# Kernel tuning notes

Measured on AMD Instinct MI355X. Metric: run time of the kernel, lower is better.

## Reference

```python
import jax, jax.numpy as jnp
import numpy as np

ALPHA = 0.1        # self.alpha in the torch module
NUM_CLASSES = 10   # predict_acc hardcodes range(10)


def _sqdist(x, centers):
    # Faithful to sum((x - c)**2, -1) but computed via the gemm identity to
    # avoid materializing the (N, K, D) broadcast the torch code creates.
    x2 = jnp.sum(x * x, axis=1, keepdims=True)          # [N, 1]
    c2 = jnp.sum(centers * centers, axis=1)             # [K]
    d = x2 + c2[None, :] - 2.0 * (x @ centers.T)        # [N, K]
    return jnp.maximum(d, 0.0)                          # clamp fp round-off


def _predict_acc(distance, y):
    n = distance.shape[0]
    y_p = jnp.argmin(distance, axis=1)                  # index[1][:, 0]
    # counts[i, c] = #points assigned to cluster i (only i < 10 matter) with label c
    onehot_cluster = (y_p[:, None] == jnp.arange(NUM_CLASSES)[None, :]).astype(jnp.float32)  # [N, 10]
    onehot_label = (y[:, None] == jnp.arange(NUM_CLASSES)[None, :]).astype(jnp.float32)      # [N, 10]
    counts = onehot_cluster.T @ onehot_label            # [10, 10]
    used = jnp.zeros((NUM_CLASSES,), dtype=bool)
    correct = jnp.float32(0.0)
    for i in range(NUM_CLASSES):
        bin_i = counts[i]
        has_points = jnp.sum(bin_i) > 0                 # empty bincount -> 'continue'
        label = jnp.argmax(bin_i)                       # first max index, like where(bin==max)[0][0]
        # quchong: recursively zero already-used labels == argmax with used masked out
        masked = jnp.where(used, 0.0, bin_i)
        label = jnp.where(used[label], jnp.argmax(masked), label)
        correct = correct + jnp.where(has_points, bin_i[label], 0.0)
        used = jnp.where(has_points, used.at[label].set(True), used)
    return correct / jnp.float32(n)


def setup_inputs() -> dict:
    key = jax.random.key(0)
    kx, ky, kc = jax.random.split(key, 3)
    N, K, D = 262144, 256, 64
    x = jax.random.normal(kx, (N, D), dtype=jnp.float32)
    y = jax.random.randint(ky, (N,), 0, 10, dtype=jnp.int64)
    centers = jax.random.normal(kc, (K, D), dtype=jnp.float32)
    return {"x": x, "y": y, "centers": centers}


def reference(x, y, centers):
    distance = _sqdist(x, centers)                      # caldis, op='l2'
    # calwei: exp(-alpha*log(d+1)) then row-normalize
    we = jnp.exp(-ALPHA * jnp.log1p(distance))
    weight = we / jnp.sum(we, axis=1, keepdims=True)
    loss = jnp.sum(weight * distance)                   # calloss
    acc = _predict_acc(distance, y)
    return (loss, acc)
```

## Files before the change

### kernel.cpp

```cpp
#include <hip/hip_runtime.h>

#define ALPHA 0.1f
#define NUM_CLASSES 10

typedef __attribute__((ext_vector_type(8))) short bf16x8;
typedef __attribute__((ext_vector_type(4))) float f32x4;


__device__ __forceinline__ unsigned pack2(float a, float b) {
    return (__float_as_uint(b) & 0xFFFF0000u) | (__float_as_uint(a) >> 16);
}
__device__ __forceinline__ float truncbf(float a) {
    return __uint_as_float(__float_as_uint(a) & 0xFFFF0000u);
}


__global__ __launch_bounds__(256) void prep_kernel(
    const float* __restrict__ centers,
    unsigned int* __restrict__ ctpk,
    float* __restrict__ c2,
    float* __restrict__ loss_acc,
    unsigned int* __restrict__ counts)
{
    const int k = threadIdx.x;
    const int cg = k >> 6, ct = (k >> 4) & 3, r = k & 15;

    float cv[64];
    float s = 0.f;
    const float4* crow = (const float4*)(centers + k * 64);
#pragma unroll
    for (int j4 = 0; j4 < 16; ++j4) {
        float4 v = crow[j4];
        cv[j4 * 4 + 0] = v.x; cv[j4 * 4 + 1] = v.y;
        cv[j4 * 4 + 2] = v.z; cv[j4 * 4 + 3] = v.w;
        s += v.x * v.x + v.y * v.y + v.z * v.z + v.w * v.w;
    }
    c2[k] = s;

    uint4* out4 = (uint4*)ctpk;
#pragma unroll
    for (int f = 0; f < 4; ++f) {
#pragma unroll
        for (int q = 0; q < 4; ++q) {
            const int cbase = (f & 1) * 32 + q * 8;
            unsigned wv[4];
#pragma unroll
            for (int j2 = 0; j2 < 4; ++j2) {
                float a = cv[cbase + j2 * 2], b = cv[cbase + j2 * 2 + 1];
                if (f >= 2) { a = a - truncbf(a); b = b - truncbf(b); }
                wv[j2] = pack2(a, b);
            }
            const int lane = q * 16 + r;
            out4[((cg * 4 + ct) * 4 + f) * 64 + lane] =
                make_uint4(wv[0], wv[1], wv[2], wv[3]);
        }
    }
    if (k < NUM_CLASSES * NUM_CLASSES) counts[k] = 0u;
    if (k == 0) loss_acc[0] = 0.f;
}


__global__ __launch_bounds__(256, 2) void dist_kernel(
    const float* __restrict__ x,
    const int*   __restrict__ y,
    const unsigned int* __restrict__ ctpk,
    const float* __restrict__ c2g,
    float* __restrict__ loss_acc,
    unsigned int* __restrict__ counts,
    int NT)
{
    __shared__ float    comb_swe[4][64];
    __shared__ float    comb_swd[4][64];
    __shared__ unsigned comb_best[4][64];

    const int tid  = threadIdx.x;
    const int cg   = tid >> 6;
    const int lane = tid & 63;
    const int q    = lane >> 4;
    const int r    = lane & 15;

    bf16x8 af[4][4];
    const uint4* cp4 = (const uint4*)ctpk;
#pragma unroll
    for (int ct = 0; ct < 4; ++ct)
#pragma unroll
        for (int f = 0; f < 4; ++f) {
            union { uint4 u; bf16x8 v; } tmp;
            tmp.u = cp4[((cg * 4 + ct) * 4 + f) * 64 + lane];
            af[ct][f] = tmp.v;
        }

    float c2r[4][4];
#pragma unroll
    for (int ct = 0; ct < 4; ++ct) {
        float4 v = *(const float4*)(c2g + cg * 64 + ct * 16 + q * 4);
        c2r[ct][0] = v.x; c2r[ct][1] = v.y; c2r[ct][2] = v.z; c2r[ct][3] = v.w;
    }

    float loss_local = 0.f;

    for (int t = blockIdx.x; t < NT; t += gridDim.x) {
        bf16x8 bh0[4], bh1[4], bl0[4], bl1[4];
        float x2v[4];
#pragma unroll
        for (int pt = 0; pt < 4; ++pt) {
            const int row = t * 64 + pt * 16 + r;
            const float4* X = (const float4*)(x + (size_t)row * 64);
            float4 v0 = X[q * 2], v1 = X[q * 2 + 1];
            float4 v2 = X[8 + q * 2], v3 = X[9 + q * 2];

            float p = v0.x * v0.x;
            p = fmaf(v0.y, v0.y, p); p = fmaf(v0.z, v0.z, p); p = fmaf(v0.w, v0.w, p);
            p = fmaf(v1.x, v1.x, p); p = fmaf(v1.y, v1.y, p); p = fmaf(v1.z, v1.z, p); p = fmaf(v1.w, v1.w, p);
            p = fmaf(v2.x, v2.x, p); p = fmaf(v2.y, v2.y, p); p = fmaf(v2.z, v2.z, p); p = fmaf(v2.w, v2.w, p);
            p = fmaf(v3.x, v3.x, p); p = fmaf(v3.y, v3.y, p); p = fmaf(v3.z, v3.z, p); p = fmaf(v3.w, v3.w, p);
            p += __shfl_xor(p, 16);
            p += __shfl_xor(p, 32);
            x2v[pt] = p;

            union { bf16x8 v; unsigned u[4]; } h0, h1, l0, l1;
            h0.u[0] = pack2(v0.x, v0.y); h0.u[1] = pack2(v0.z, v0.w);
            h0.u[2] = pack2(v1.x, v1.y); h0.u[3] = pack2(v1.z, v1.w);
            h1.u[0] = pack2(v2.x, v2.y); h1.u[1] = pack2(v2.z, v2.w);
            h1.u[2] = pack2(v3.x, v3.y); h1.u[3] = pack2(v3.z, v3.w);
            l0.u[0] = pack2(v0.x - truncbf(v0.x), v0.y - truncbf(v0.y));
            l0.u[1] = pack2(v0.z - truncbf(v0.z), v0.w - truncbf(v0.w));
            l0.u[2] = pack2(v1.x - truncbf(v1.x), v1.y - truncbf(v1.y));
            l0.u[3] = pack2(v1.z - truncbf(v1.z), v1.w - truncbf(v1.w));
            l1.u[0] = pack2(v2.x - truncbf(v2.x), v2.y - truncbf(v2.y));
            l1.u[1] = pack2(v2.z - truncbf(v2.z), v2.w - truncbf(v2.w));
            l1.u[2] = pack2(v3.x - truncbf(v3.x), v3.y - truncbf(v3.y));
            l1.u[3] = pack2(v3.z - truncbf(v3.z), v3.w - truncbf(v3.w));
            bh0[pt] = h0.v; bh1[pt] = h1.v; bl0[pt] = l0.v; bl1[pt] = l1.v;
        }

        f32x4 acc[4][4];
#pragma unroll
        for (int ct = 0; ct < 4; ++ct)
#pragma unroll
            for (int pt = 0; pt < 4; ++pt) acc[ct][pt] = (f32x4){0.f, 0.f, 0.f, 0.f};

#pragma unroll
        for (int ct = 0; ct < 4; ++ct)
#pragma unroll
            for (int pt = 0; pt < 4; ++pt) {
                f32x4 a = acc[ct][pt];
                a = __builtin_amdgcn_mfma_f32_16x16x32_bf16(af[ct][0], bh0[pt], a, 0, 0, 0);
                a = __builtin_amdgcn_mfma_f32_16x16x32_bf16(af[ct][1], bh1[pt], a, 0, 0, 0);
                a = __builtin_amdgcn_mfma_f32_16x16x32_bf16(af[ct][2], bh0[pt], a, 0, 0, 0);
                a = __builtin_amdgcn_mfma_f32_16x16x32_bf16(af[ct][3], bh1[pt], a, 0, 0, 0);
                a = __builtin_amdgcn_mfma_f32_16x16x32_bf16(af[ct][0], bl0[pt], a, 0, 0, 0);
                a = __builtin_amdgcn_mfma_f32_16x16x32_bf16(af[ct][1], bl1[pt], a, 0, 0, 0);
                acc[ct][pt] = a;
            }

#pragma unroll
        for (int pt = 0; pt < 4; ++pt) {
            float swe = 0.f, swd = 0.f;
            unsigned best = 0xFFFFFFFFu;
            const float x2p = x2v[pt];
#pragma unroll
            for (int ct = 0; ct < 4; ++ct) {
#pragma unroll
                for (int reg = 0; reg < 4; ++reg) {
                    float d = fmaf(-2.f, acc[ct][pt][reg], x2p + c2r[ct][reg]);
                    d = fmaxf(d, 0.f);
                    const unsigned kid = (unsigned)(cg * 64 + ct * 16 + q * 4 + reg);
                    unsigned u = (__float_as_uint(d) & 0xFFFFFF00u) | kid;
                    best = min(best, u);
                    float wg = exp2f(-ALPHA * __log2f(1.f + d));
                    swe += wg;
                    swd = fmaf(wg, d, swd);
                }
            }
            swe += __shfl_xor(swe, 16); swe += __shfl_xor(swe, 32);
            swd += __shfl_xor(swd, 16); swd += __shfl_xor(swd, 32);
            best = min(best, (unsigned)__shfl_xor((int)best, 16));
            best = min(best, (unsigned)__shfl_xor((int)best, 32));
            if (q == 0) {
                comb_swe[cg][pt * 16 + r] = swe;
                comb_swd[cg][pt * 16 + r] = swd;
                comb_best[cg][pt * 16 + r] = best;
            }
        }
        __syncthreads();

        if (tid < 64) {
            float SWE = comb_swe[0][tid], SWD = comb_swd[0][tid];
            unsigned BEST = comb_best[0][tid];
#pragma unroll
            for (int g = 1; g < 4; ++g) {
                SWE += comb_swe[g][tid];
                SWD += comb_swd[g][tid];
                BEST = min(BEST, comb_best[g][tid]);
            }
            loss_local += SWD / SWE;
            const unsigned bk = BEST & 0xFFu;
            if (bk < NUM_CLASSES) {
                const int lbl = y[t * 64 + tid];
                atomicAdd(&counts[bk * NUM_CLASSES + lbl], 1u);
            }
        }
        __syncthreads();
    }

    if (cg == 0) {
        float v = loss_local;
#pragma unroll
        for (int o = 32; o > 0; o >>= 1) v += __shfl_down(v, o);
        if (lane == 0) atomicAdd(loss_acc, v);
    }
}


__global__ void finalize_kernel(
    const float* __restrict__ loss_acc,
    const unsigned int* __restrict__ counts,
    float* __restrict__ out,
    int N)
{
    if (threadIdx.x == 0 && blockIdx.x == 0) {
        float c[NUM_CLASSES][NUM_CLASSES];
        for (int i = 0; i < NUM_CLASSES; ++i)
            for (int j = 0; j < NUM_CLASSES; ++j)
                c[i][j] = (float)counts[i * NUM_CLASSES + j];

        bool used[NUM_CLASSES];
        for (int i = 0; i < NUM_CLASSES; ++i) used[i] = false;

        float correct = 0.f;
        for (int i = 0; i < NUM_CLASSES; ++i) {
            float rowsum = 0.f;
            for (int j = 0; j < NUM_CLASSES; ++j) rowsum += c[i][j];
            bool has_points = rowsum > 0.f;

            int label = 0;
            float mx = c[i][0];
            for (int j = 1; j < NUM_CLASSES; ++j)
                if (c[i][j] > mx) { mx = c[i][j]; label = j; }

            if (used[label]) {
                float mm = used[0] ? 0.f : c[i][0];
                int l2 = 0;
                for (int j = 1; j < NUM_CLASSES; ++j) {
                    float v = used[j] ? 0.f : c[i][j];
                    if (v > mm) { mm = v; l2 = j; }
                }
                label = l2;
            }

            if (has_points) {
                correct += c[i][label];
                used[label] = true;
            }
        }
        out[0] = loss_acc[0];
        out[1] = correct / (float)N;
    }
}


extern "C" void kernel_launch(void* const* d_in, const int* in_sizes, int n_in,
                              void* d_out, int out_size, void* d_ws, size_t ws_size,
                              hipStream_t stream)
{
    const float* x       = (const float*)d_in[0];
    const int*   y       = (const int*)d_in[1];
    const float* centers = (const float*)d_in[2];
    float* out = (float*)d_out;

    const int N  = in_sizes[0] / 64;
    const int NT = N / 64;

    unsigned int* ctpk   = (unsigned int*)d_ws;
    float* c2            = (float*)((char*)d_ws + 65536);
    float* loss          = (float*)((char*)d_ws + 66560);
    unsigned int* counts = (unsigned int*)((char*)d_ws + 66564);

    prep_kernel<<<1, 256, 0, stream>>>(centers, ctpk, c2, loss, counts);

    int grid = 512;
    if (grid > NT) grid = NT;
    dist_kernel<<<grid, 256, 0, stream>>>(x, y, ctpk, c2, loss, counts, NT);

    finalize_kernel<<<1, 64, 0, stream>>>(loss, counts, out, N);
}
```

Baseline: 161.0 us.

## Fuse center prep into distance kernel and split centers across eight waves

Drops the separate prep kernel. Each block now computes the center norms and the bf16 hi/lo center fragments itself, and counters are zeroed with a memset. Blocks grow to 512 threads: eight waves each own 32 centers, while four waves load and split the x tile and stage it through shared memory for all eight. The aim is to remove a launch, cut per-wave register pressure and raise occupancy. The cost is that every block re-reads the centers, and there is an extra LDS round trip plus a barrier per tile.

```diff
diff --git a/kernel.cpp b/kernel.cpp
--- a/kernel.cpp
+++ b/kernel.cpp
@@ -15,96 +15,75 @@
 }
 
 
-__global__ __launch_bounds__(256) void prep_kernel(
-    const float* __restrict__ centers,
-    unsigned int* __restrict__ ctpk,
-    float* __restrict__ c2,
-    float* __restrict__ loss_acc,
-    unsigned int* __restrict__ counts)
-{
-    const int k = threadIdx.x;
-    const int cg = k >> 6, ct = (k >> 4) & 3, r = k & 15;
-
-    float cv[64];
-    float s = 0.f;
-    const float4* crow = (const float4*)(centers + k * 64);
-#pragma unroll
-    for (int j4 = 0; j4 < 16; ++j4) {
-        float4 v = crow[j4];
-        cv[j4 * 4 + 0] = v.x; cv[j4 * 4 + 1] = v.y;
-        cv[j4 * 4 + 2] = v.z; cv[j4 * 4 + 3] = v.w;
-        s += v.x * v.x + v.y * v.y + v.z * v.z + v.w * v.w;
-    }
-    c2[k] = s;
-
-    uint4* out4 = (uint4*)ctpk;
-#pragma unroll
-    for (int f = 0; f < 4; ++f) {
-#pragma unroll
-        for (int q = 0; q < 4; ++q) {
-            const int cbase = (f & 1) * 32 + q * 8;
-            unsigned wv[4];
-#pragma unroll
-            for (int j2 = 0; j2 < 4; ++j2) {
-                float a = cv[cbase + j2 * 2], b = cv[cbase + j2 * 2 + 1];
-                if (f >= 2) { a = a - truncbf(a); b = b - truncbf(b); }
-                wv[j2] = pack2(a, b);
-            }
-            const int lane = q * 16 + r;
-            out4[((cg * 4 + ct) * 4 + f) * 64 + lane] =
-                make_uint4(wv[0], wv[1], wv[2], wv[3]);
-        }
-    }
-    if (k < NUM_CLASSES * NUM_CLASSES) counts[k] = 0u;
-    if (k == 0) loss_acc[0] = 0.f;
-}
-
-
-__global__ __launch_bounds__(256, 2) void dist_kernel(
+__global__ __launch_bounds__(512, 4) void dist_kernel(
     const float* __restrict__ x,
     const int*   __restrict__ y,
-    const unsigned int* __restrict__ ctpk,
-    const float* __restrict__ c2g,
+    const float* __restrict__ centers,
     float* __restrict__ loss_acc,
     unsigned int* __restrict__ counts,
     int NT)
 {
-    __shared__ float    comb_swe[4][64];
-    __shared__ float    comb_swd[4][64];
-    __shared__ unsigned comb_best[4][64];
+    __shared__ __align__(16) char bstage[4 * 4 * 64 * 16];
+    __shared__ float x2s[64];
+    __shared__ float c2s[256];
+    __shared__ float    comb_swe[8][64];
+    __shared__ float    comb_swd[8][64];
+    __shared__ unsigned comb_best[8][64];
 
     const int tid  = threadIdx.x;
-    const int cg   = tid >> 6;
+    const int w    = tid >> 6;
     const int lane = tid & 63;
     const int q    = lane >> 4;
     const int r    = lane & 15;
 
-    bf16x8 af[4][4];
-    const uint4* cp4 = (const uint4*)ctpk;
-#pragma unroll
-    for (int ct = 0; ct < 4; ++ct)
-#pragma unroll
-        for (int f = 0; f < 4; ++f) {
-            union { uint4 u; bf16x8 v; } tmp;
-            tmp.u = cp4[((cg * 4 + ct) * 4 + f) * 64 + lane];
-            af[ct][f] = tmp.v;
-        }
-
-    float c2r[4][4];
-#pragma unroll
-    for (int ct = 0; ct < 4; ++ct) {
-        float4 v = *(const float4*)(c2g + cg * 64 + ct * 16 + q * 4);
+    if (tid < 256) {
+        const float4* crow = (const float4*)(centers + tid * 64);
+        float s = 0.f;
+#pragma unroll
+        for (int j = 0; j < 16; ++j) {
+            float4 v = crow[j];
+            s = fmaf(v.x, v.x, s); s = fmaf(v.y, v.y, s);
+            s = fmaf(v.z, v.z, s); s = fmaf(v.w, v.w, s);
+        }
+        c2s[tid] = s;
+    }
+
+    bf16x8 af[2][4];
+#pragma unroll
+    for (int ct = 0; ct < 2; ++ct) {
+        const int row = w * 32 + ct * 16 + r;
+        const float4* C = (const float4*)(centers + (size_t)row * 64);
+        float4 v0 = C[q * 2], v1 = C[q * 2 + 1];
+        float4 v2 = C[8 + q * 2], v3 = C[9 + q * 2];
+        union { bf16x8 v; unsigned u[4]; } h0, h1, l0, l1;
+        h0.u[0] = pack2(v0.x, v0.y); h0.u[1] = pack2(v0.z, v0.w);
+        h0.u[2] = pack2(v1.x, v1.y); h0.u[3] = pack2(v1.z, v1.w);
+        h1.u[0] = pack2(v2.x, v2.y); h1.u[1] = pack2(v2.z, v2.w);
+        h1.u[2] = pack2(v3.x, v3.y); h1.u[3] = pack2(v3.z, v3.w);
+        l0.u[0] = pack2(v0.x - truncbf(v0.x), v0.y - truncbf(v0.y));
+        l0.u[1] = pack2(v0.z - truncbf(v0.z), v0.w - truncbf(v0.w));
+        l0.u[2] = pack2(v1.x - truncbf(v1.x), v1.y - truncbf(v1.y));
+        l0.u[3] = pack2(v1.z - truncbf(v1.z), v1.w - truncbf(v1.w));
+        l1.u[0] = pack2(v2.x - truncbf(v2.x), v2.y - truncbf(v2.y));
+        l1.u[1] = pack2(v2.z - truncbf(v2.z), v2.w - truncbf(v2.w));
+        l1.u[2] = pack2(v3.x - truncbf(v3.x), v3.y - truncbf(v3.y));
+        l1.u[3] = pack2(v3.z - truncbf(v3.z), v3.w - truncbf(v3.w));
+        af[ct][0] = h0.v; af[ct][1] = h1.v; af[ct][2] = l0.v; af[ct][3] = l1.v;
+    }
+    __syncthreads();
+
+    float c2r[2][4];
+#pragma unroll
+    for (int ct = 0; ct < 2; ++ct) {
+        float4 v = *(const float4*)(c2s + w * 32 + ct * 16 + q * 4);
         c2r[ct][0] = v.x; c2r[ct][1] = v.y; c2r[ct][2] = v.z; c2r[ct][3] = v.w;
     }
 
     float loss_local = 0.f;
 
     for (int t = blockIdx.x; t < NT; t += gridDim.x) {
-        bf16x8 bh0[4], bh1[4], bl0[4], bl1[4];
-        float x2v[4];
-#pragma unroll
-        for (int pt = 0; pt < 4; ++pt) {
-            const int row = t * 64 + pt * 16 + r;
+        if (w < 4) {
+            const int row = t * 64 + w * 16 + r;
             const float4* X = (const float4*)(x + (size_t)row * 64);
             float4 v0 = X[q * 2], v1 = X[q * 2 + 1];
             float4 v2 = X[8 + q * 2], v3 = X[9 + q * 2];
@@ -116,9 +95,9 @@
             p = fmaf(v3.x, v3.x, p); p = fmaf(v3.y, v3.y, p); p = fmaf(v3.z, v3.z, p); p = fmaf(v3.w, v3.w, p);
             p += __shfl_xor(p, 16);
             p += __shfl_xor(p, 32);
-            x2v[pt] = p;
-
-            union { bf16x8 v; unsigned u[4]; } h0, h1, l0, l1;
+            if (q == 0) x2s[w * 16 + r] = p;
+
+            union { bf16x8 v; uint4 u4; unsigned u[4]; } h0, h1, l0, l1;
             h0.u[0] = pack2(v0.x, v0.y); h0.u[1] = pack2(v0.z, v0.w);
             h0.u[2] = pack2(v1.x, v1.y); h0.u[3] = pack2(v1.z, v1.w);
             h1.u[0] = pack2(v2.x, v2.y); h1.u[1] = pack2(v2.z, v2.w);
@@ -131,41 +110,44 @@
             l1.u[1] = pack2(v2.z - truncbf(v2.z), v2.w - truncbf(v2.w));
             l1.u[2] = pack2(v3.x - truncbf(v3.x), v3.y - truncbf(v3.y));
             l1.u[3] = pack2(v3.z - truncbf(v3.z), v3.w - truncbf(v3.w));
-            bh0[pt] = h0.v; bh1[pt] = h1.v; bl0[pt] = l0.v; bl1[pt] = l1.v;
-        }
-
-        f32x4 acc[4][4];
-#pragma unroll
-        for (int ct = 0; ct < 4; ++ct)
-#pragma unroll
-            for (int pt = 0; pt < 4; ++pt) acc[ct][pt] = (f32x4){0.f, 0.f, 0.f, 0.f};
-
-#pragma unroll
-        for (int ct = 0; ct < 4; ++ct)
-#pragma unroll
-            for (int pt = 0; pt < 4; ++pt) {
-                f32x4 a = acc[ct][pt];
-                a = __builtin_amdgcn_mfma_f32_16x16x32_bf16(af[ct][0], bh0[pt], a, 0, 0, 0);
-                a = __builtin_amdgcn_mfma_f32_16x16x32_bf16(af[ct][1], bh1[pt], a, 0, 0, 0);
-                a = __builtin_amdgcn_mfma_f32_16x16x32_bf16(af[ct][2], bh0[pt], a, 0, 0, 0);
-                a = __builtin_amdgcn_mfma_f32_16x16x32_bf16(af[ct][3], bh1[pt], a, 0, 0, 0);
-                a = __builtin_amdgcn_mfma_f32_16x16x32_bf16(af[ct][0], bl0[pt], a, 0, 0, 0);
-                a = __builtin_amdgcn_mfma_f32_16x16x32_bf16(af[ct][1], bl1[pt], a, 0, 0, 0);
-                acc[ct][pt] = a;
-            }
+            *(uint4*)(bstage + (((w * 4 + 0) * 64 + lane) << 4)) = h0.u4;
+            *(uint4*)(bstage + (((w * 4 + 1) * 64 + lane) << 4)) = h1.u4;
+            *(uint4*)(bstage + (((w * 4 + 2) * 64 + lane) << 4)) = l0.u4;
+            *(uint4*)(bstage + (((w * 4 + 3) * 64 + lane) << 4)) = l1.u4;
+        }
+        __syncthreads();
 
 #pragma unroll
         for (int pt = 0; pt < 4; ++pt) {
+            union { uint4 u4; bf16x8 v; } b0, b1, b2, b3;
+            b0.u4 = *(const uint4*)(bstage + (((pt * 4 + 0) * 64 + lane) << 4));
+            b1.u4 = *(const uint4*)(bstage + (((pt * 4 + 1) * 64 + lane) << 4));
+            b2.u4 = *(const uint4*)(bstage + (((pt * 4 + 2) * 64 + lane) << 4));
+            b3.u4 = *(const uint4*)(bstage + (((pt * 4 + 3) * 64 + lane) << 4));
+            const float x2p = x2s[pt * 16 + r];
+
+            f32x4 acc[2];
+#pragma unroll
+            for (int ct = 0; ct < 2; ++ct) {
+                f32x4 a = (f32x4){0.f, 0.f, 0.f, 0.f};
+                a = __builtin_amdgcn_mfma_f32_16x16x32_bf16(af[ct][0], b0.v, a, 0, 0, 0);
+                a = __builtin_amdgcn_mfma_f32_16x16x32_bf16(af[ct][1], b1.v, a, 0, 0, 0);
+                a = __builtin_amdgcn_mfma_f32_16x16x32_bf16(af[ct][2], b0.v, a, 0, 0, 0);
+                a = __builtin_amdgcn_mfma_f32_16x16x32_bf16(af[ct][3], b1.v, a, 0, 0, 0);
+                a = __builtin_amdgcn_mfma_f32_16x16x32_bf16(af[ct][0], b2.v, a, 0, 0, 0);
+                a = __builtin_amdgcn_mfma_f32_16x16x32_bf16(af[ct][1], b3.v, a, 0, 0, 0);
+                acc[ct] = a;
+            }
+
             float swe = 0.f, swd = 0.f;
             unsigned best = 0xFFFFFFFFu;
-            const float x2p = x2v[pt];
-#pragma unroll
-            for (int ct = 0; ct < 4; ++ct) {
+#pragma unroll
+            for (int ct = 0; ct < 2; ++ct) {
 #pragma unroll
                 for (int reg = 0; reg < 4; ++reg) {
-                    float d = fmaf(-2.f, acc[ct][pt][reg], x2p + c2r[ct][reg]);
+                    float d = fmaf(-2.f, acc[ct][reg], x2p + c2r[ct][reg]);
                     d = fmaxf(d, 0.f);
-                    const unsigned kid = (unsigned)(cg * 64 + ct * 16 + q * 4 + reg);
+                    const unsigned kid = (unsigned)(w * 32 + ct * 16 + q * 4 + reg);
                     unsigned u = (__float_as_uint(d) & 0xFFFFFF00u) | kid;
                     best = min(best, u);
                     float wg = exp2f(-ALPHA * __log2f(1.f + d));
@@ -178,9 +160,9 @@
             best = min(best, (unsigned)__shfl_xor((int)best, 16));
             best = min(best, (unsigned)__shfl_xor((int)best, 32));
             if (q == 0) {
-                comb_swe[cg][pt * 16 + r] = swe;
-                comb_swd[cg][pt * 16 + r] = swd;
-                comb_best[cg][pt * 16 + r] = best;
+                comb_swe[w][pt * 16 + r] = swe;
+                comb_swd[w][pt * 16 + r] = swd;
+                comb_best[w][pt * 16 + r] = best;
             }
         }
         __syncthreads();
@@ -189,7 +171,7 @@
             float SWE = comb_swe[0][tid], SWD = comb_swd[0][tid];
             unsigned BEST = comb_best[0][tid];
 #pragma unroll
-            for (int g = 1; g < 4; ++g) {
+            for (int g = 1; g < 8; ++g) {
                 SWE += comb_swe[g][tid];
                 SWD += comb_swd[g][tid];
                 BEST = min(BEST, comb_best[g][tid]);
@@ -201,10 +183,9 @@
                 atomicAdd(&counts[bk * NUM_CLASSES + lbl], 1u);
             }
         }
-        __syncthreads();
-    }
-
-    if (cg == 0) {
+    }
+
+    if (w == 0) {
         float v = loss_local;
 #pragma unroll
         for (int o = 32; o > 0; o >>= 1) v += __shfl_down(v, o);
@@ -272,16 +253,14 @@
     const int N  = in_sizes[0] / 64;
     const int NT = N / 64;
 
-    unsigned int* ctpk   = (unsigned int*)d_ws;
-    float* c2            = (float*)((char*)d_ws + 65536);
-    float* loss          = (float*)((char*)d_ws + 66560);
-    unsigned int* counts = (unsigned int*)((char*)d_ws + 66564);
-
-    prep_kernel<<<1, 256, 0, stream>>>(centers, ctpk, c2, loss, counts);
+    float* loss          = (float*)d_ws;
+    unsigned int* counts = (unsigned int*)((char*)d_ws + 4);
+
+    hipMemsetAsync(d_ws, 0, 512, stream);
 
     int grid = 512;
     if (grid > NT) grid = NT;
-    dist_kernel<<<grid, 256, 0, stream>>>(x, y, ctpk, c2, loss, counts, NT);
+    dist_kernel<<<grid, 512, 0, stream>>>(x, y, centers, loss, counts, NT);
 
     finalize_kernel<<<1, 64, 0, stream>>>(loss, counts, out, N);
 }
```

Result: faster. 153.3 us (-4.8%).

## Give each wave whole rows, stream centers per tile, fuse finalize into last block

Applied to the files above, without the earlier changes.

Reorganizes the distance kernel so each wave owns 64 rows and loops over all 256 centers. It streams the packed center fragments from global/L2 with one-tile-ahead prefetch, instead of keeping a wave-specific quarter of the centers resident in registers. This removes the shared-memory cross-wave combine and both __syncthreads per tile, allows higher occupancy (launch bounds 4), and launches one block per 256 rows rather than a persistent grid. The finalize kernel is folded into the last-finishing block through a done counter and threadfence, saving one launch. The cost is repeated center loads per wave, plus a risk of lower MFMA density per loaded fragment.

```diff
diff --git a/kernel.cpp b/kernel.cpp
--- a/kernel.cpp
+++ b/kernel.cpp
@@ -20,10 +20,11 @@
     unsigned int* __restrict__ ctpk,
     float* __restrict__ c2,
     float* __restrict__ loss_acc,
-    unsigned int* __restrict__ counts)
+    unsigned int* __restrict__ counts,
+    unsigned int* __restrict__ done)
 {
     const int k = threadIdx.x;
-    const int cg = k >> 6, ct = (k >> 4) & 3, r = k & 15;
+    const int ct = k >> 4, r = k & 15;
 
     float cv[64];
     float s = 0.f;
@@ -50,61 +51,43 @@
                 if (f >= 2) { a = a - truncbf(a); b = b - truncbf(b); }
                 wv[j2] = pack2(a, b);
             }
-            const int lane = q * 16 + r;
-            out4[((cg * 4 + ct) * 4 + f) * 64 + lane] =
+            out4[(ct * 4 + f) * 64 + q * 16 + r] =
                 make_uint4(wv[0], wv[1], wv[2], wv[3]);
         }
     }
     if (k < NUM_CLASSES * NUM_CLASSES) counts[k] = 0u;
-    if (k == 0) loss_acc[0] = 0.f;
-}
-
-
-__global__ __launch_bounds__(256, 2) void dist_kernel(
+    if (k == 100) loss_acc[0] = 0.f;
+    if (k == 101) done[0] = 0u;
+}
+
+
+__global__ __launch_bounds__(256, 4) void dist_kernel(
     const float* __restrict__ x,
     const int*   __restrict__ y,
-    const unsigned int* __restrict__ ctpk,
+    const uint4* __restrict__ ctpk4,
     const float* __restrict__ c2g,
     float* __restrict__ loss_acc,
     unsigned int* __restrict__ counts,
-    int NT)
+    unsigned int* __restrict__ done,
+    float* __restrict__ out,
+    int N)
 {
-    __shared__ float    comb_swe[4][64];
-    __shared__ float    comb_swd[4][64];
-    __shared__ unsigned comb_best[4][64];
-
     const int tid  = threadIdx.x;
-    const int cg   = tid >> 6;
+    const int w    = tid >> 6;
     const int lane = tid & 63;
     const int q    = lane >> 4;
     const int r    = lane & 15;
-
-    bf16x8 af[4][4];
-    const uint4* cp4 = (const uint4*)ctpk;
-#pragma unroll
-    for (int ct = 0; ct < 4; ++ct)
-#pragma unroll
-        for (int f = 0; f < 4; ++f) {
-            union { uint4 u; bf16x8 v; } tmp;
-            tmp.u = cp4[((cg * 4 + ct) * 4 + f) * 64 + lane];
-            af[ct][f] = tmp.v;
-        }
-
-    float c2r[4][4];
-#pragma unroll
-    for (int ct = 0; ct < 4; ++ct) {
-        float4 v = *(const float4*)(c2g + cg * 64 + ct * 16 + q * 4);
-        c2r[ct][0] = v.x; c2r[ct][1] = v.y; c2r[ct][2] = v.z; c2r[ct][3] = v.w;
-    }
+    const int base = blockIdx.x * 256 + w * 64;
 
     float loss_local = 0.f;
 
-    for (int t = blockIdx.x; t < NT; t += gridDim.x) {
-        bf16x8 bh0[4], bh1[4], bl0[4], bl1[4];
-        float x2v[4];
-#pragma unroll
-        for (int pt = 0; pt < 4; ++pt) {
-            const int row = t * 64 + pt * 16 + r;
+#pragma unroll 1
+    for (int h = 0; h < 2; ++h) {
+        bf16x8 bh0[2], bh1[2], bl0[2], bl1[2];
+        float x2p[2];
+#pragma unroll
+        for (int s = 0; s < 2; ++s) {
+            const int row = base + h * 32 + s * 16 + r;
             const float4* X = (const float4*)(x + (size_t)row * 64);
             float4 v0 = X[q * 2], v1 = X[q * 2 + 1];
             float4 v2 = X[8 + q * 2], v3 = X[9 + q * 2];
@@ -116,7 +99,7 @@
             p = fmaf(v3.x, v3.x, p); p = fmaf(v3.y, v3.y, p); p = fmaf(v3.z, v3.z, p); p = fmaf(v3.w, v3.w, p);
             p += __shfl_xor(p, 16);
             p += __shfl_xor(p, 32);
-            x2v[pt] = p;
+            x2p[s] = p;
 
             union { bf16x8 v; unsigned u[4]; } h0, h1, l0, l1;
             h0.u[0] = pack2(v0.x, v0.y); h0.u[1] = pack2(v0.z, v0.w);
@@ -131,131 +114,127 @@
             l1.u[1] = pack2(v2.z - truncbf(v2.z), v2.w - truncbf(v2.w));
             l1.u[2] = pack2(v3.x - truncbf(v3.x), v3.y - truncbf(v3.y));
             l1.u[3] = pack2(v3.z - truncbf(v3.z), v3.w - truncbf(v3.w));
-            bh0[pt] = h0.v; bh1[pt] = h1.v; bl0[pt] = l0.v; bl1[pt] = l1.v;
-        }
-
-        f32x4 acc[4][4];
-#pragma unroll
-        for (int ct = 0; ct < 4; ++ct)
-#pragma unroll
-            for (int pt = 0; pt < 4; ++pt) acc[ct][pt] = (f32x4){0.f, 0.f, 0.f, 0.f};
-
-#pragma unroll
-        for (int ct = 0; ct < 4; ++ct)
-#pragma unroll
-            for (int pt = 0; pt < 4; ++pt) {
-                f32x4 a = acc[ct][pt];
-                a = __builtin_amdgcn_mfma_f32_16x16x32_bf16(af[ct][0], bh0[pt], a, 0, 0, 0);
-                a = __builtin_amdgcn_mfma_f32_16x16x32_bf16(af[ct][1], bh1[pt], a, 0, 0, 0);
-                a = __builtin_amdgcn_mfma_f32_16x16x32_bf16(af[ct][2], bh0[pt], a, 0, 0, 0);
-                a = __builtin_amdgcn_mfma_f32_16x16x32_bf16(af[ct][3], bh1[pt], a, 0, 0, 0);
-                a = __builtin_amdgcn_mfma_f32_16x16x32_bf16(af[ct][0], bl0[pt], a, 0, 0, 0);
-                a = __builtin_amdgcn_mfma_f32_16x16x32_bf16(af[ct][1], bl1[pt], a, 0, 0, 0);
-                acc[ct][pt] = a;
-            }
-
-#pragma unroll
-        for (int pt = 0; pt < 4; ++pt) {
-            float swe = 0.f, swd = 0.f;
-            unsigned best = 0xFFFFFFFFu;
-            const float x2p = x2v[pt];
-#pragma unroll
-            for (int ct = 0; ct < 4; ++ct) {
+            bh0[s] = h0.v; bh1[s] = h1.v; bl0[s] = l0.v; bl1[s] = l1.v;
+        }
+
+        float swe[2] = {0.f, 0.f}, swd[2] = {0.f, 0.f};
+        unsigned best[2] = {0xFFFFFFFFu, 0xFFFFFFFFu};
+
+        uint4 na0 = ctpk4[0 * 64 + lane], na1 = ctpk4[1 * 64 + lane];
+        uint4 na2 = ctpk4[2 * 64 + lane], na3 = ctpk4[3 * 64 + lane];
+        float4 nc2 = *(const float4*)(c2g + q * 4);
+
+#pragma unroll 1
+        for (int ct = 0; ct < 16; ++ct) {
+            union { uint4 u; bf16x8 v; } af0, af1, af2, af3;
+            af0.u = na0; af1.u = na1; af2.u = na2; af3.u = na3;
+            const float c2a0 = nc2.x, c2a1 = nc2.y, c2a2 = nc2.z, c2a3 = nc2.w;
+
+            if (ct < 15) {
+                const int nb = (ct + 1) * 4 * 64;
+                na0 = ctpk4[nb + 0 * 64 + lane];
+                na1 = ctpk4[nb + 1 * 64 + lane];
+                na2 = ctpk4[nb + 2 * 64 + lane];
+                na3 = ctpk4[nb + 3 * 64 + lane];
+                nc2 = *(const float4*)(c2g + (ct + 1) * 16 + q * 4);
+            }
+
+            f32x4 acc[2];
+#pragma unroll
+            for (int s = 0; s < 2; ++s) {
+                f32x4 a = (f32x4){0.f, 0.f, 0.f, 0.f};
+                a = __builtin_amdgcn_mfma_f32_16x16x32_bf16(af0.v, bh0[s], a, 0, 0, 0);
+                a = __builtin_amdgcn_mfma_f32_16x16x32_bf16(af1.v, bh1[s], a, 0, 0, 0);
+                a = __builtin_amdgcn_mfma_f32_16x16x32_bf16(af2.v, bh0[s], a, 0, 0, 0);
+                a = __builtin_amdgcn_mfma_f32_16x16x32_bf16(af3.v, bh1[s], a, 0, 0, 0);
+                a = __builtin_amdgcn_mfma_f32_16x16x32_bf16(af0.v, bl0[s], a, 0, 0, 0);
+                a = __builtin_amdgcn_mfma_f32_16x16x32_bf16(af1.v, bl1[s], a, 0, 0, 0);
+                acc[s] = a;
+            }
+
+#pragma unroll
+            for (int s = 0; s < 2; ++s) {
+                const float x2v = x2p[s];
+                const float c2a[4] = {c2a0, c2a1, c2a2, c2a3};
 #pragma unroll
                 for (int reg = 0; reg < 4; ++reg) {
-                    float d = fmaf(-2.f, acc[ct][pt][reg], x2p + c2r[ct][reg]);
+                    float d = fmaf(-2.f, acc[s][reg], x2v + c2a[reg]);
                     d = fmaxf(d, 0.f);
-                    const unsigned kid = (unsigned)(cg * 64 + ct * 16 + q * 4 + reg);
+                    const unsigned kid = (unsigned)(ct * 16 + q * 4 + reg);
                     unsigned u = (__float_as_uint(d) & 0xFFFFFF00u) | kid;
-                    best = min(best, u);
+                    best[s] = min(best[s], u);
                     float wg = exp2f(-ALPHA * __log2f(1.f + d));
-                    swe += wg;
-                    swd = fmaf(wg, d, swd);
-                }
-            }
-            swe += __shfl_xor(swe, 16); swe += __shfl_xor(swe, 32);
-            swd += __shfl_xor(swd, 16); swd += __shfl_xor(swd, 32);
-            best = min(best, (unsigned)__shfl_xor((int)best, 16));
-            best = min(best, (unsigned)__shfl_xor((int)best, 32));
+                    swe[s] += wg;
+                    swd[s] = fmaf(wg, d, swd[s]);
+                }
+            }
+        }
+
+#pragma unroll
+        for (int s = 0; s < 2; ++s) {
+            float SWE = swe[s], SWD = swd[s];
+            unsigned B = best[s];
+            SWE += __shfl_xor(SWE, 16); SWE += __shfl_xor(SWE, 32);
+            SWD += __shfl_xor(SWD, 16); SWD += __shfl_xor(SWD, 32);
+            B = min(B, (unsigned)__shfl_xor((int)B, 16));
+            B = min(B, (unsigned)__shfl_xor((int)B, 32));
             if (q == 0) {
-                comb_swe[cg][pt * 16 + r] = swe;
-                comb_swd[cg][pt * 16 + r] = swd;
-                comb_best[cg][pt * 16 + r] = best;
-            }
-        }
-        __syncthreads();
-
-        if (tid < 64) {
-            float SWE = comb_swe[0][tid], SWD = comb_swd[0][tid];
-            unsigned BEST = comb_best[0][tid];
-#pragma unroll
-            for (int g = 1; g < 4; ++g) {
-                SWE += comb_swe[g][tid];
-                SWD += comb_swd[g][tid];
-                BEST = min(BEST, comb_best[g][tid]);
-            }
-            loss_local += SWD / SWE;
-            const unsigned bk = BEST & 0xFFu;
-            if (bk < NUM_CLASSES) {
-                const int lbl = y[t * 64 + tid];
-                atomicAdd(&counts[bk * NUM_CLASSES + lbl], 1u);
-            }
-        }
-        __syncthreads();
-    }
-
-    if (cg == 0) {
-        float v = loss_local;
-#pragma unroll
-        for (int o = 32; o > 0; o >>= 1) v += __shfl_down(v, o);
-        if (lane == 0) atomicAdd(loss_acc, v);
-    }
-}
-
-
-__global__ void finalize_kernel(
-    const float* __restrict__ loss_acc,
-    const unsigned int* __restrict__ counts,
-    float* __restrict__ out,
-    int N)
-{
-    if (threadIdx.x == 0 && blockIdx.x == 0) {
-        float c[NUM_CLASSES][NUM_CLASSES];
-        for (int i = 0; i < NUM_CLASSES; ++i)
-            for (int j = 0; j < NUM_CLASSES; ++j)
-                c[i][j] = (float)counts[i * NUM_CLASSES + j];
-
-        bool used[NUM_CLASSES];
-        for (int i = 0; i < NUM_CLASSES; ++i) used[i] = false;
-
-        float correct = 0.f;
-        for (int i = 0; i < NUM_CLASSES; ++i) {
-            float rowsum = 0.f;
-            for (int j = 0; j < NUM_CLASSES; ++j) rowsum += c[i][j];
-            bool has_points = rowsum > 0.f;
-
-            int label = 0;
-            float mx = c[i][0];
-            for (int j = 1; j < NUM_CLASSES; ++j)
-                if (c[i][j] > mx) { mx = c[i][j]; label = j; }
-
-            if (used[label]) {
-                float mm = used[0] ? 0.f : c[i][0];
-                int l2 = 0;
-                for (int j = 1; j < NUM_CLASSES; ++j) {
-                    float v = used[j] ? 0.f : c[i][j];
-                    if (v > mm) { mm = v; l2 = j; }
-                }
-                label = l2;
-            }
-
-            if (has_points) {
-                correct += c[i][label];
-                used[label] = true;
-            }
-        }
-        out[0] = loss_acc[0];
-        out[1] = correct / (float)N;
+                loss_local += SWD / SWE;
+                const unsigned bk = B & 0xFFu;
+                if (bk < NUM_CLASSES) {
+                    const int lbl = y[base + h * 32 + s * 16 + r];
+                    atomicAdd(&counts[bk * NUM_CLASSES + lbl], 1u);
+                }
+            }
+        }
+    }
+
+    float v = loss_local;
+#pragma unroll
+    for (int o = 32; o > 0; o >>= 1) v += __shfl_down(v, o);
+    if (lane == 0) atomicAdd(loss_acc, v);
+
+    __syncthreads();
+    if (tid == 0) {
+        __threadfence();
+        if (atomicAdd(done, 1u) == gridDim.x - 1) {
+            __threadfence();
+            float c[NUM_CLASSES][NUM_CLASSES];
+            for (int i = 0; i < NUM_CLASSES; ++i)
+                for (int j = 0; j < NUM_CLASSES; ++j)
+                    c[i][j] = (float)atomicAdd(&counts[i * NUM_CLASSES + j], 0u);
+            const float L = atomicAdd(loss_acc, 0.f);
+
+            bool used[NUM_CLASSES];
+            for (int i = 0; i < NUM_CLASSES; ++i) used[i] = false;
+            float correct = 0.f;
+            for (int i = 0; i < NUM_CLASSES; ++i) {
+                float rowsum = 0.f;
+                for (int j = 0; j < NUM_CLASSES; ++j) rowsum += c[i][j];
+                const bool has_points = rowsum > 0.f;
+
+                int label = 0;
+                float mx = c[i][0];
+                for (int j = 1; j < NUM_CLASSES; ++j)
+                    if (c[i][j] > mx) { mx = c[i][j]; label = j; }
+
+                if (used[label]) {
+                    float mm = used[0] ? 0.f : c[i][0];
+                    int l2 = 0;
+                    for (int j = 1; j < NUM_CLASSES; ++j) {
+                        float vv = used[j] ? 0.f : c[i][j];
+                        if (vv > mm) { mm = vv; l2 = j; }
+                    }
+                    label = l2;
+                }
+                if (has_points) {
+                    correct += c[i][label];
+                    used[label] = true;
+                }
+            }
+            out[0] = L;
+            out[1] = correct / (float)N;
+        }
     }
 }
 
@@ -269,19 +248,17 @@
     const float* centers = (const float*)d_in[2];
     float* out = (float*)d_out;
 
-    const int N  = in_sizes[0] / 64;
-    const int NT = N / 64;
+    const int N = in_sizes[0] / 64;
 
     unsigned int* ctpk   = (unsigned int*)d_ws;
     float* c2            = (float*)((char*)d_ws + 65536);
     float* loss          = (float*)((char*)d_ws + 66560);
     unsigned int* counts = (unsigned int*)((char*)d_ws + 66564);
-
-    prep_kernel<<<1, 256, 0, stream>>>(centers, ctpk, c2, loss, counts);
-
-    int grid = 512;
-    if (grid > NT) grid = NT;
-    dist_kernel<<<grid, 256, 0, stream>>>(x, y, ctpk, c2, loss, counts, NT);
-
-    finalize_kernel<<<1, 64, 0, stream>>>(loss, counts, out, N);
-}
+    unsigned int* done   = (unsigned int*)((char*)d_ws + 66964);
+
+    prep_kernel<<<1, 256, 0, stream>>>(centers, ctpk, c2, loss, counts, done);
+
+    const int grid = N / 256;
+    dist_kernel<<<grid, 256, 0, stream>>>(x, y, (const uint4*)ctpk, c2,
+                                          loss, counts, done, out, N);
+}
```

New measurement: 204.3 us. +26.9%, slower.
